# Performance work log

Hardware: AMD Instinct MI355X
Metric: run time of the kernel (lower is better)

## Reference

```python
import jax, jax.numpy as jnp
import numpy as np

B = 128; D = 192; DI = 384; DS = 16; DR = 12; L = 17; DEPTH = 12
NH = 8; HD = D // NH; NCLS = 10; EPS = 1e-5


def setup_inputs() -> dict:
    key = jax.random.key(0)
    ks = iter(jax.random.split(key, 128))
    def rn(shape, s=0.02):
        return jax.random.normal(next(ks), shape, dtype=jnp.float32) * s
    inp = {"x": jax.random.normal(next(ks), (B, 8, 224, 16), dtype=jnp.float32)}
    inp["t_patch_w"] = rn((D, 8, 14, 16)); inp["t_patch_b"] = jnp.zeros((D,), jnp.float32)
    inp["f_patch_w"] = rn((D, 8, 224, 1)); inp["f_patch_b"] = jnp.zeros((D,), jnp.float32)
    inp["t_tok"] = rn((1, 1, D)); inp["f_tok"] = rn((1, 1, D))
    inp["t_pos"] = rn((1, L, D)); inp["f_pos"] = rn((1, L, D))
    for p in ("t", "f"):
        inp[p + "_norm_w"] = jnp.ones((DEPTH, D), jnp.float32)
        inp[p + "_in_proj"] = rn((DEPTH, 2 * DI, D))
        inp[p + "_conv_w"] = rn((DEPTH, DI, 4), 0.3)
        inp[p + "_conv_b"] = jnp.zeros((DEPTH, DI), jnp.float32)
        inp[p + "_x_proj"] = rn((DEPTH, DR + 2 * DS, DI))
        inp[p + "_dt_w"] = rn((DEPTH, DI, DR))
        inp[p + "_dt_b"] = rn((DEPTH, DI), 0.5)
        A = jnp.tile(jnp.arange(1, DS + 1, dtype=jnp.float32)[None, None, :], (DEPTH, DI, 1))
        inp[p + "_A_log"] = jnp.log(A)
        inp[p + "_D"] = jnp.ones((DEPTH, DI), jnp.float32)
        inp[p + "_out_proj"] = rn((DEPTH, D, DI))
    inp["att_t_w"] = rn((4, D, D)); inp["att_t_b"] = jnp.zeros((4, D), jnp.float32)
    inp["att_tf_w"] = rn((4, D, D)); inp["att_tf_b"] = jnp.zeros((4, D), jnp.float32)
    inp["cls1_w"] = rn((512, D)); inp["cls1_b"] = jnp.zeros((512,), jnp.float32)
    inp["cls2_w"] = rn((NCLS, 512)); inp["cls2_b"] = jnp.zeros((NCLS,), jnp.float32)
    inp["pos1_w"] = rn((512, D)); inp["pos1_b"] = jnp.zeros((512,), jnp.float32)
    inp["pos2_w"] = rn((3, 512)); inp["pos2_b"] = jnp.zeros((3,), jnp.float32)
    return inp


def silu(x):
    return x * jax.nn.sigmoid(x)


def patch_embed(x, w, b, stride):
    # Conv2d VALID, then flatten(2).transpose(1,2) -> (B, num_patch, D)
    y = jax.lax.conv_general_dilated(x, w, window_strides=stride, padding="VALID",
                                     dimension_numbers=("NCHW", "OIHW", "NCHW"))
    y = y + b[None, :, None, None]
    Bb, C, H, W = y.shape
    return y.reshape(Bb, C, H * W).transpose(0, 2, 1)


def rmsnorm(x, w):
    return x * jax.lax.rsqrt(jnp.mean(x * x, -1, keepdims=True) + EPS) * w


def mamba_mixer(x, in_proj, conv_w, conv_b, x_proj, dt_w, dt_b, A_log, Dp, out_proj):
    Bb, Ll, _ = x.shape
    xz = x @ in_proj.T                         # (B,L,2*DI)
    xx, z = xz[..., :DI], xz[..., DI:]
    # depthwise causal conv, kernel 4, left pad 3
    xp = jnp.pad(xx, ((0, 0), (3, 0), (0, 0)))
    xx = sum(xp[:, k:k + Ll, :] * conv_w[:, k] for k in range(4)) + conv_b
    xx = silu(xx)                              # (B,L,DI)
    dbl = xx @ x_proj.T                        # (B,L,DR+2*DS)
    dt = jax.nn.softplus(dbl[..., :DR] @ dt_w.T + dt_b)     # (B,L,DI)
    Bm = dbl[..., DR:DR + DS]                  # (B,L,DS)
    Cm = dbl[..., DR + DS:]                    # (B,L,DS)
    A = -jnp.exp(A_log)                        # (DI,DS)
    dA = jnp.exp(dt[..., None] * A)            # (B,L,DI,DS)
    dBx = dt[..., None] * Bm[:, :, None, :] * xx[..., None]

    def step(h, inputs):
        dA_l, dBx_l, C_l = inputs
        h = dA_l * h + dBx_l
        y = jnp.einsum("bcn,bn->bc", h, C_l)
        return h, y

    h0 = jnp.zeros((Bb, DI, DS), x.dtype)
    _, ys = jax.lax.scan(step, h0, (dA.transpose(1, 0, 2, 3),
                                    dBx.transpose(1, 0, 2, 3),
                                    Cm.transpose(1, 0, 2)))
    y = ys.transpose(1, 0, 2) + Dp * xx
    y = y * silu(z)
    return y @ out_proj.T


def backbone(x, norm_w, in_proj, conv_w, conv_b, x_proj, dt_w, dt_b, A_log, Dp, out_proj):
    residual = None
    for i in range(DEPTH):
        residual = x if residual is None else residual + x
        h = rmsnorm(residual, norm_w[i])
        x = mamba_mixer(h, in_proj[i], conv_w[i], conv_b[i], x_proj[i],
                        dt_w[i], dt_b[i], A_log[i], Dp[i], out_proj[i])
    return x


def cross_attn(q, kv, w, b):
    Bb, Lq, _ = q.shape; Lk = kv.shape[1]
    qh = (q @ w[0].T + b[0]).reshape(Bb, Lq, NH, HD).transpose(0, 2, 1, 3)
    kh = (kv @ w[1].T + b[1]).reshape(Bb, Lk, NH, HD).transpose(0, 2, 1, 3)
    vh = (kv @ w[2].T + b[2]).reshape(Bb, Lk, NH, HD).transpose(0, 2, 1, 3)
    att = jax.nn.softmax(jnp.einsum("bhqd,bhkd->bhqk", qh, kh) / np.float32(np.sqrt(HD)), axis=-1)
    o = jnp.einsum("bhqk,bhkd->bhqd", att, vh).transpose(0, 2, 1, 3).reshape(Bb, Lq, D)
    return o @ w[3].T + b[3]


def reference(x, t_patch_w, t_patch_b, f_patch_w, f_patch_b, t_tok, f_tok, t_pos, f_pos,
              t_norm_w, t_in_proj, t_conv_w, t_conv_b, t_x_proj, t_dt_w, t_dt_b, t_A_log, t_D, t_out_proj,
              f_norm_w, f_in_proj, f_conv_w, f_conv_b, f_x_proj, f_dt_w, f_dt_b, f_A_log, f_D, f_out_proj,
              att_t_w, att_t_b, att_tf_w, att_tf_b,
              cls1_w, cls1_b, cls2_w, cls2_b, pos1_w, pos1_b, pos2_w, pos2_b):
    Bb = x.shape[0]
    t = patch_embed(x, t_patch_w, t_patch_b, (14, 1))     # (B,16,D)
    f = patch_embed(x, f_patch_w, f_patch_b, (1, 1))      # (B,16,D)
    t = jnp.concatenate([t, jnp.broadcast_to(t_tok, (Bb, 1, D))], axis=1)
    f = jnp.concatenate([f, jnp.broadcast_to(f_tok, (Bb, 1, D))], axis=1)
    t = t + t_pos
    f = f + f_pos
    t = backbone(t, t_norm_w, t_in_proj, t_conv_w, t_conv_b, t_x_proj,
                 t_dt_w, t_dt_b, t_A_log, t_D, t_out_proj)
    f = backbone(f, f_norm_w, f_in_proj, f_conv_w, f_conv_b, f_x_proj,
                 f_dt_w, f_dt_b, f_A_log, f_D, f_out_proj)
    t1 = cross_attn(t, f, att_t_w, att_t_b)
    fusion = cross_attn(t1, f, att_tf_w, att_tf_b)
    fusion = t + fusion
    feat = fusion[:, -1, :]
    cls = jax.nn.relu(feat @ cls1_w.T + cls1_b) @ cls2_w.T + cls2_b
    pos = jax.nn.relu(feat @ pos1_w.T + pos1_b) @ pos2_w.T + pos2_b
    return (cls, pos)
```

## Files before the change

### kernel.cpp

```cpp
#include <hip/hip_runtime.h>
#include <math.h>

#define NB 128
#define SEQ 17
#define DM 192
#define DI 384
#define DEPTH 12
#define ROW (SEQ*DM)
#define NROWS 4352
#define N192 (NROWS*DM)
#define C1IP (DEPTH*2*DI*DM)
#define C2OP (DEPTH*DM*DI)
#define KEMB 1792
#define CEMB_STRIDE 786432

typedef __attribute__((ext_vector_type(8))) short bf16x8;
typedef __attribute__((ext_vector_type(4))) float f32x4;

struct MambaW {
  const float* norm_w;
  const float* in_proj;
  const float* conv_w;
  const float* conv_b;
  const float* x_proj;
  const float* dt_w;
  const float* dt_b;
  const float* A_log;
  const float* D;
  const float* out_proj;
};

__device__ __forceinline__ float dot4(float4 a, float4 b) {
  return a.x*b.x + a.y*b.y + a.z*b.z + a.w*b.w;
}
__device__ __forceinline__ unsigned short f2bf(float f) {
  unsigned int u = __float_as_uint(f);
  u += 0x7FFFu + ((u >> 16) & 1u);
  return (unsigned short)(u >> 16);
}
__device__ __forceinline__ float bf2f(unsigned short h) {
  return __uint_as_float(((unsigned int)h) << 16);
}
__device__ __forceinline__ void split2(float v, unsigned short& h, unsigned short& l) {
  h = f2bf(v);
  l = f2bf(v - bf2f(h));
}

__global__ __launch_bounds__(256) void decomp_kernel(
    const float* __restrict__ s0, const float* __restrict__ s1,
    unsigned short* __restrict__ hi, unsigned short* __restrict__ lo, int nquads)
{
  const float* s = blockIdx.y ? s1 : s0;
  size_t base = (size_t)blockIdx.y * nquads;
  for (size_t i = (size_t)blockIdx.x*256 + threadIdx.x; i < (size_t)nquads;
       i += (size_t)gridDim.x*256) {
    float4 v = ((const float4*)s)[i];
    ushort4 h, l;
    split2(v.x, h.x, l.x); split2(v.y, h.y, l.y);
    split2(v.z, h.z, l.z); split2(v.w, h.w, l.w);
    ((ushort4*)hi)[base + i] = h;
    ((ushort4*)lo)[base + i] = l;
  }
}

__global__ __launch_bounds__(256) void prep_kernel(
    const float* __restrict__ x, float* __restrict__ Af)
{
  const int t = threadIdx.x;
  const int b = blockIdx.x >> 3, c = blockIdx.x & 7;
  const float* xp = x + (size_t)(b*8 + c)*3584;
  __shared__ float ts[16][225];
  for (int idx = t; idx < 3584; idx += 256)
    ts[idx & 15][idx >> 4] = xp[idx];
  __syncthreads();
  for (int i4 = t; i4 < 896; i4 += 256) {
    const int p = i4 / 56, r4 = (i4 - p*56)*4;
    float4 v;
    v.x = ts[p][r4]; v.y = ts[p][r4+1]; v.z = ts[p][r4+2]; v.w = ts[p][r4+3];
    *(float4*)&Af[(size_t)(b*16 + p)*KEMB + c*224 + r4] = v;
  }
}

__global__ __launch_bounds__(256) void gemm_embed(
    const float* __restrict__ x, const float* __restrict__ Af,
    const float* __restrict__ Wt, const float* __restrict__ Wf,
    float* __restrict__ C)
{
  const int t = threadIdx.x;
  const int mt = blockIdx.x, nt = blockIdx.y, kz = blockIdx.z;
  __shared__ float As[32][68];
  __shared__ float Bs[32][68];

  const float* Wsel = (nt < 32 ? Wt : Wf) + (size_t)(mt*64)*KEMB;

  const int srow = t >> 2;
  const int a8   = t & 3;
  const int sw   = (a8 & 1) << 4;
  const int colA = srow ^ sw;

  const int tn = t & 15;
  const int tm = t >> 4;
  float acc[4][4];
#pragma unroll
  for (int i = 0; i < 4; ++i)
#pragma unroll
    for (int j = 0; j < 4; ++j) acc[i][j] = 0.f;

  const int kbase = kz*448;
  const float* xrowbase = nullptr;
  const float* afrow    = nullptr;
  if (nt < 32) {
    const int r = nt*64 + srow;
    const int b = r >> 4, p = r & 15;
    xrowbase = x + (size_t)(b*8)*3584 + p*224 + a8*8;
  } else {
    const int r = (nt - 32)*64 + srow;
    afrow = Af + (size_t)r*KEMB + kbase + a8*8;
  }
  const float* brow = Wsel + (size_t)srow*KEMB + kbase + a8*8;

  int cblk = kz*2, rr = 0;
  float4 pa0, pa1, pb0, pb1;
  {
    const float* ar = (nt < 32) ? (xrowbase + (size_t)cblk*3584 + rr) : afrow;
    pa0 = *(const float4*)(ar + 0);
    pa1 = *(const float4*)(ar + 4);
    pb0 = *(const float4*)(brow + 0);
    pb1 = *(const float4*)(brow + 4);
  }

  for (int kt = 0; kt < 448; kt += 32) {
    As[a8*8+0][colA]=pa0.x; As[a8*8+1][colA]=pa0.y;
    As[a8*8+2][colA]=pa0.z; As[a8*8+3][colA]=pa0.w;
    As[a8*8+4][colA]=pa1.x; As[a8*8+5][colA]=pa1.y;
    As[a8*8+6][colA]=pa1.z; As[a8*8+7][colA]=pa1.w;
    Bs[a8*8+0][colA]=pb0.x; Bs[a8*8+1][colA]=pb0.y;
    Bs[a8*8+2][colA]=pb0.z; Bs[a8*8+3][colA]=pb0.w;
    Bs[a8*8+4][colA]=pb1.x; Bs[a8*8+5][colA]=pb1.y;
    Bs[a8*8+6][colA]=pb1.z; Bs[a8*8+7][colA]=pb1.w;
    __syncthreads();
    if (kt + 32 < 448) {
      rr += 32; if (rr == 224) { rr = 0; ++cblk; }
      const float* ar = (nt < 32) ? (xrowbase + (size_t)cblk*3584 + rr)
                                  : (afrow + kt + 32);
      pa0 = *(const float4*)(ar + 0);
      pa1 = *(const float4*)(ar + 4);
      const float* br = brow + kt + 32;
      pb0 = *(const float4*)(br + 0);
      pb1 = *(const float4*)(br + 4);
    }
#pragma unroll
    for (int kk = 0; kk < 32; ++kk) {
      const int xr = ((kk >> 3) & 1) << 4;
      float a[4], b[4];
      *(float4*)&a[0] = *(const float4*)&As[kk][(tn*4) ^ xr];
      *(float4*)&b[0] = *(const float4*)&Bs[kk][(tm*4) ^ xr];
#pragma unroll
      for (int i = 0; i < 4; ++i)
#pragma unroll
        for (int j = 0; j < 4; ++j) acc[i][j] = fmaf(a[i], b[j], acc[i][j]);
    }
    __syncthreads();
  }

  float* Cb = C + (size_t)kz*CEMB_STRIDE
            + (size_t)(nt*64 + tn*4)*DM + mt*64 + tm*4;
#pragma unroll
  for (int i = 0; i < 4; ++i)
    *(float4*)(Cb + (size_t)i*DM) = *(float4*)&acc[i][0];
}

template<int MT>
__global__ __launch_bounds__(256) void gemm_mfma(
    const unsigned short* __restrict__ Ahi, const unsigned short* __restrict__ Alo, int lda,
    const unsigned short* __restrict__ BtHi, const unsigned short* __restrict__ BtLo,
    const unsigned short* __restrict__ BfHi, const unsigned short* __restrict__ BfLo,
    int ldb, int kchunk, float* __restrict__ C, int ldc, long ckstride)
{
  const int t = threadIdx.x;
  const int mt = blockIdx.x, nt = blockIdx.y, kz = blockIdx.z;
  __shared__ alignas(16) unsigned short sAh[64*40], sAl[64*40];
  __shared__ alignas(16) unsigned short sBh[MT*40], sBl[MT*40];

  const bool isT = (nt < 34);
  const unsigned short* aH = Ahi + (size_t)(nt*64)*lda + kz*kchunk;
  const unsigned short* aL = Alo + (size_t)(nt*64)*lda + kz*kchunk;
  const unsigned short* bH = (isT ? BtHi : BfHi) + (size_t)(mt*MT)*ldb + kz*kchunk;
  const unsigned short* bL = (isT ? BtLo : BfLo) + (size_t)(mt*MT)*ldb + kz*kchunk;

  const int wave = t >> 6, lane = t & 63;
  const int arow = wave*16 + (lane & 15);
  const int kb   = (lane >> 4) * 8;

  f32x4 acc[MT/16];
#pragma unroll
  for (int mb = 0; mb < MT/16; ++mb) acc[mb] = (f32x4){0.f, 0.f, 0.f, 0.f};

  const int srow = t >> 2, sseg = (t & 3) * 8;

  for (int kt = 0; kt < kchunk; kt += 32) {
    __syncthreads();
    *(uint4*)(sAh + srow*40 + sseg) = *(const uint4*)(aH + (size_t)srow*lda + kt + sseg);
    *(uint4*)(sAl + srow*40 + sseg) = *(const uint4*)(aL + (size_t)srow*lda + kt + sseg);
#pragma unroll
    for (int rep = 0; rep < MT/64; ++rep) {
      int r2 = rep*64 + srow;
      *(uint4*)(sBh + r2*40 + sseg) = *(const uint4*)(bH + (size_t)r2*ldb + kt + sseg);
      *(uint4*)(sBl + r2*40 + sseg) = *(const uint4*)(bL + (size_t)r2*ldb + kt + sseg);
    }
    __syncthreads();
    bf16x8 ah = *(const bf16x8*)(sAh + arow*40 + kb);
    bf16x8 al = *(const bf16x8*)(sAl + arow*40 + kb);
#pragma unroll
    for (int mb = 0; mb < MT/16; ++mb) {
      bf16x8 bh = *(const bf16x8*)(sBh + (mb*16 + (lane & 15))*40 + kb);
      bf16x8 bl = *(const bf16x8*)(sBl + (mb*16 + (lane & 15))*40 + kb);
      acc[mb] = __builtin_amdgcn_mfma_f32_16x16x32_bf16(al, bh, acc[mb], 0, 0, 0);
      acc[mb] = __builtin_amdgcn_mfma_f32_16x16x32_bf16(ah, bl, acc[mb], 0, 0, 0);
      acc[mb] = __builtin_amdgcn_mfma_f32_16x16x32_bf16(ah, bh, acc[mb], 0, 0, 0);
    }
  }

  float* Cb = C + (long)kz*ckstride
            + (size_t)(nt*64 + wave*16 + (lane >> 4)*4)*ldc + mt*MT + (lane & 15);
#pragma unroll
  for (int mb = 0; mb < MT/16; ++mb)
#pragma unroll
    for (int r = 0; r < 4; ++r)
      Cb[(size_t)r*ldc + mb*16] = acc[mb][r];
}

__global__ __launch_bounds__(192) void embed_fin_kernel(
    const float* __restrict__ Cg,
    const float* __restrict__ bT, const float* __restrict__ posT,
    const float* __restrict__ tokT, const float* __restrict__ nwT,
    const float* __restrict__ bF, const float* __restrict__ posF,
    const float* __restrict__ tokF, const float* __restrict__ nwF,
    float* __restrict__ res,
    unsigned short* __restrict__ hHi, unsigned short* __restrict__ hLo)
{
  const int d = threadIdx.x;
  const int sb = blockIdx.x;
  const int is_f = sb >> 7, b = sb & 127;
  const float* bias = is_f ? bF : bT;
  const float* pos  = is_f ? posF : posT;
  const float* tok  = is_f ? tokF : tokT;
  const float* nw   = is_f ? nwF : nwT;
  __shared__ float sq[SEQ*192];
  __shared__ float pt[SEQ*8];
  __shared__ float sc[SEQ];

  float v[SEQ];
  const float* Crow = Cg + ((size_t)is_f*2048 + (size_t)b*16)*DM + d;
  const float add = bias[d];
#pragma unroll
  for (int l = 0; l < 16; ++l) {
    v[l] = (Crow[l*DM] + Crow[(size_t)CEMB_STRIDE + l*DM])
         + (Crow[(size_t)2*CEMB_STRIDE + l*DM] + Crow[(size_t)3*CEMB_STRIDE + l*DM])
         + add + pos[l*DM + d];
    sq[l*192 + d] = v[l]*v[l];
  }
  v[16] = tok[d] + pos[16*DM + d];
  sq[16*192 + d] = v[16]*v[16];
  __syncthreads();
  if (d < 136) {
    int l = d >> 3, j = d & 7;
    float s = 0.f;
#pragma unroll
    for (int q = 0; q < 24; ++q) s += sq[l*192 + j + 8*q];
    pt[d] = s;
  }
  __syncthreads();
  if (d < SEQ) {
    float s = 0.f;
#pragma unroll
    for (int j = 0; j < 8; ++j) s += pt[d*8 + j];
    sc[d] = rsqrtf(s*(1.0f/192.0f) + 1e-5f);
  }
  __syncthreads();
  float nwd = nw[d];
#pragma unroll
  for (int l = 0; l < SEQ; ++l) {
    size_t idx = ((size_t)sb*SEQ + l)*DM + d;
    res[idx] = v[l];
    unsigned short h, lo_;
    split2(v[l]*sc[l]*nwd, h, lo_);
    hHi[idx] = h; hLo[idx] = lo_;
  }
}

__global__ __launch_bounds__(384) void mid_kernel(
    const float* __restrict__ xzg,
    unsigned short* __restrict__ yHi, unsigned short* __restrict__ yLo,
    MambaW wt, MambaW wf, int layer)
{
  const int t = threadIdx.x;
  const int sb = blockIdx.x;
  const MambaW W = (sb >= NB) ? wf : wt;
  __shared__ alignas(16) float lds_xx[SEQ*388];
  __shared__ alignas(16) float lds_dbl[748];
  const size_t nb = (size_t)sb*SEQ;

  float xr[SEQ];
  {
    const float4 cw = ((const float4*)(W.conv_w + (size_t)layer*DI*4))[t];
    const float cb = W.conv_b[layer*DI + t];
    float p0 = 0.f, p1 = 0.f, p2 = 0.f;
#pragma unroll
    for (int l = 0; l < SEQ; ++l) {
      float xz = xzg[(nb + l)*768 + t];
      float v = cb + xz*cw.w + p0*cw.z + p1*cw.y + p2*cw.x;
      p2 = p1; p1 = p0; p0 = xz;
      v = v / (1.f + __expf(-v));
      xr[l] = v;
      lds_xx[l*388 + t] = v;
    }
  }
  __syncthreads();

  {
    const float* XP = W.x_proj + (size_t)layer*44*DI;
#pragma unroll
    for (int rep = 0; rep < 2; ++rep) {
      int o = t + rep*384;
      if (o < 748) {
        int j = o / 17, l = o - j*17;
        const float4* wr = (const float4*)(XP + j*DI);
        const float4* xv4 = (const float4*)lds_xx + l*97;
        float a = 0.f;
        for (int k4 = 0; k4 < 96; ++k4) a += dot4(xv4[k4], wr[k4]);
        lds_dbl[l*44 + j] = a;
      }
    }
  }
  __syncthreads();

  {
    const int c = t;
    const float* dwr = W.dt_w + (size_t)layer*DI*12 + c*12;
    float w0[12];
#pragma unroll
    for (int r = 0; r < 12; ++r) w0[r] = dwr[r];
    const float dtb = W.dt_b[layer*DI + c];
    const float4* alr = (const float4*)(W.A_log + (size_t)layer*DI*16) + c*4;
    float Av[16];
#pragma unroll
    for (int q = 0; q < 4; ++q) {
      float4 a4 = alr[q];
      Av[q*4+0] = -__expf(a4.x); Av[q*4+1] = -__expf(a4.y);
      Av[q*4+2] = -__expf(a4.z); Av[q*4+3] = -__expf(a4.w);
    }
    const float Dp = W.D[layer*DI + c];
    float hst[16];
#pragma unroll
    for (int n = 0; n < 16; ++n) hst[n] = 0.f;
    for (int l = 0; l < SEQ; ++l) {
      float a = dtb;
#pragma unroll
      for (int r = 0; r < 12; ++r) a += lds_dbl[l*44 + r]*w0[r];
      float dt = (a > 20.f) ? a : log1pf(__expf(a));
      float xv = xr[l];
      const float4* dbv = (const float4*)(lds_dbl + l*44 + 12);
      float4 Bq[4], Cq[4];
      Bq[0]=dbv[0]; Bq[1]=dbv[1]; Bq[2]=dbv[2]; Bq[3]=dbv[3];
      Cq[0]=dbv[4]; Cq[1]=dbv[5]; Cq[2]=dbv[6]; Cq[3]=dbv[7];
      const float* Bs = (const float*)Bq;
      const float* Cs = (const float*)Cq;
      float y = 0.f;
      float dbx = dt * xv;
#pragma unroll
      for (int n = 0; n < 16; ++n) {
        float dA = __expf(dt * Av[n]);
        float hn = dA*hst[n] + dbx*Bs[n];
        hst[n] = hn;
        y += hn*Cs[n];
      }
      y += Dp * xv;
      float zv = xzg[(nb + l)*768 + DI + c];
      y *= zv / (1.f + __expf(-zv));
      unsigned short h, lo_;
      split2(y, h, lo_);
      size_t idx = (nb + l)*DI + c;
      yHi[idx] = h; yLo[idx] = lo_;
    }
  }
}

__global__ __launch_bounds__(192) void fuse_kernel(
    const float* __restrict__ part, float* __restrict__ res,
    unsigned short* __restrict__ hHi, unsigned short* __restrict__ hLo,
    float* __restrict__ xfin,
    const float* __restrict__ nwT, const float* __restrict__ nwF,
    int layer, int last)
{
  const int d = threadIdx.x;
  const int sb = blockIdx.x;
  const size_t nb = (size_t)sb*SEQ;
  __shared__ float sq[SEQ*192];
  __shared__ float pt[SEQ*8];
  __shared__ float sc[SEQ];

  float v[SEQ];
#pragma unroll
  for (int l = 0; l < SEQ; ++l) {
    size_t idx = (nb + l)*DM + d;
    float s = part[idx] + part[(size_t)N192 + idx];
    if (!last) {
      s += res[idx];
      res[idx] = s;
      v[l] = s;
      sq[l*192 + d] = s*s;
    } else {
      xfin[idx] = s;
    }
  }
  if (last) return;
  __syncthreads();
  if (d < 136) {
    int l = d >> 3, j = d & 7;
    float s = 0.f;
#pragma unroll
    for (int q = 0; q < 24; ++q) s += sq[l*192 + j + 8*q];
    pt[d] = s;
  }
  __syncthreads();
  if (d < SEQ) {
    float s = 0.f;
#pragma unroll
    for (int j = 0; j < 8; ++j) s += pt[d*8 + j];
    sc[d] = rsqrtf(s*(1.0f/192.0f) + 1e-5f);
  }
  __syncthreads();
  const float* nw = ((sb < NB) ? nwT : nwF) + (size_t)(layer + 1)*DM;
  float nwd = nw[d];
#pragma unroll
  for (int l = 0; l < SEQ; ++l) {
    unsigned short h, lo_;
    split2(v[l]*sc[l]*nwd, h, lo_);
    size_t idx = (nb + l)*DM + d;
    hHi[idx] = h; hLo[idx] = lo_;
  }
}

__global__ __launch_bounds__(256, 3) void gemm_kv(
    const float* __restrict__ A, int lda, int ktot,
    const float* __restrict__ Bt, const float* __restrict__ Bf, int ldb,
    const float* __restrict__ bias1, const float* __restrict__ bias2,
    float* __restrict__ C, int ldc)
{
  const int t  = threadIdx.x;
  const int mt = blockIdx.x, nt = blockIdx.y;
  __shared__ float As[32][132];
  __shared__ float Bs[32][100];

  int pass = mt >> 2, kv = (mt >> 1) & 1, half = mt & 1;
  const float* Bp = (pass ? Bf : Bt) + (size_t)(1+kv)*DM*DM + (size_t)(half*96)*ldb;
  const float* bp = (pass ? bias2 : bias1) + (1+kv)*DM + half*96;
  const float* Ap = A + (size_t)(nt*128)*lda;

  const int tn = t & 15, tm = t >> 4;
  float acc[8][6];
#pragma unroll
  for (int i = 0; i < 8; ++i)
#pragma unroll
    for (int j = 0; j < 6; ++j) acc[i][j] = 0.f;

  const int srow = t >> 1;
  const int skl  = (t & 1) * 16;

  for (int kt = 0; kt < ktot; kt += 32) {
    __syncthreads();
    {
      const float* ar = Ap + (size_t)srow*lda + kt + skl;
      float4 v0 = *(const float4*)(ar + 0);
      float4 v1 = *(const float4*)(ar + 4);
      float4 v2 = *(const float4*)(ar + 8);
      float4 v3 = *(const float4*)(ar + 12);
      As[skl+ 0][srow]=v0.x; As[skl+ 1][srow]=v0.y; As[skl+ 2][srow]=v0.z; As[skl+ 3][srow]=v0.w;
      As[skl+ 4][srow]=v1.x; As[skl+ 5][srow]=v1.y; As[skl+ 6][srow]=v1.z; As[skl+ 7][srow]=v1.w;
      As[skl+ 8][srow]=v2.x; As[skl+ 9][srow]=v2.y; As[skl+10][srow]=v2.z; As[skl+11][srow]=v2.w;
      As[skl+12][srow]=v3.x; As[skl+13][srow]=v3.y; As[skl+14][srow]=v3.z; As[skl+15][srow]=v3.w;
    }
    if (srow < 96) {
      const float* br = Bp + (size_t)srow*ldb + kt + skl;
      float4 v0 = *(const float4*)(br + 0);
      float4 v1 = *(const float4*)(br + 4);
      float4 v2 = *(const float4*)(br + 8);
      float4 v3 = *(const float4*)(br + 12);
      Bs[skl+ 0][srow]=v0.x; Bs[skl+ 1][srow]=v0.y; Bs[skl+ 2][srow]=v0.z; Bs[skl+ 3][srow]=v0.w;
      Bs[skl+ 4][srow]=v1.x; Bs[skl+ 5][srow]=v1.y; Bs[skl+ 6][srow]=v1.z; Bs[skl+ 7][srow]=v1.w;
      Bs[skl+ 8][srow]=v2.x; Bs[skl+ 9][srow]=v2.y; Bs[skl+10][srow]=v2.z; Bs[skl+11][srow]=v2.w;
      Bs[skl+12][srow]=v3.x; Bs[skl+13][srow]=v3.y; Bs[skl+14][srow]=v3.z; Bs[skl+15][srow]=v3.w;
    }
    __syncthreads();
#pragma unroll
    for (int kk = 0; kk < 32; ++kk) {
      float a[8], b[6];
      *(float4*)&a[0] = *(const float4*)&As[kk][tn*4];
      *(float4*)&a[4] = *(const float4*)&As[kk][64 + tn*4];
      *(float2*)&b[0] = *(const float2*)&Bs[kk][tm*6];
      *(float2*)&b[2] = *(const float2*)&Bs[kk][tm*6+2];
      *(float2*)&b[4] = *(const float2*)&Bs[kk][tm*6+4];
#pragma unroll
      for (int i = 0; i < 8; ++i)
#pragma unroll
        for (int j = 0; j < 6; ++j) acc[i][j] = fmaf(a[i], b[j], acc[i][j]);
    }
  }

  float* Cb = C + (size_t)(nt*128)*ldc + mt*96;
#pragma unroll
  for (int ni = 0; ni < 8; ++ni) {
    int n = (ni < 4) ? tn*4 + ni : 64 + tn*4 + (ni - 4);
    float* cr = Cb + (size_t)n*ldc;
#pragma unroll
    for (int j = 0; j < 6; ++j) cr[tm*6 + j] = acc[ni][j] + bp[tm*6 + j];
  }
}

__device__ __forceinline__ void coop_gemv192(
    const float* __restrict__ W, const float* __restrict__ bias,
    const float* __restrict__ xv, float* __restrict__ y,
    const float* __restrict__ addv, int nout, int relu,
    float* __restrict__ wbuf, float* __restrict__ pt, int t)
{
  float4 pv[12];
#pragma unroll
  for (int i = 0; i < 12; ++i) pv[i] = *(const float4*)(W + (t + i*256)*4);
  for (int d0 = 0; d0 < nout; d0 += 64) {
#pragma unroll
    for (int i = 0; i < 12; ++i) {
      const int idx = (t + i*256)*4;
      const int r = idx/192, c = idx - r*192;
      float* wb = wbuf + r*193 + c;
      wb[0]=pv[i].x; wb[1]=pv[i].y; wb[2]=pv[i].z; wb[3]=pv[i].w;
    }
    __syncthreads();
    if (d0 + 64 < nout) {
      const float* nsrc = W + (size_t)(d0+64)*192;
#pragma unroll
      for (int i = 0; i < 12; ++i) pv[i] = *(const float4*)(nsrc + (t + i*256)*4);
    }
    {
      const int ol = t & 63, ks = t >> 6;
      const float* wr = wbuf + ol*193 + ks*48;
      const float* xr = xv + ks*48;
      float a = 0.f;
#pragma unroll
      for (int k = 0; k < 48; ++k) a = fmaf(wr[k], xr[k], a);
      pt[ks*64 + ol] = a;
    }
    __syncthreads();
    if (t < 64) {
      float s = (pt[t] + pt[64+t]) + (pt[128+t] + pt[192+t]) + bias[d0+t];
      if (addv) s += addv[d0+t];
      if (relu) s = fmaxf(s, 0.f);
      y[d0+t] = s;
    }
    __syncthreads();
  }
}

__global__ __launch_bounds__(256) void attn_core_kernel(
    const float* __restrict__ xfin, const float* __restrict__ kvg,
    const float* __restrict__ w1, const float* __restrict__ b1,
    const float* __restrict__ w2, const float* __restrict__ b2,
    const float* __restrict__ c1w, const float* __restrict__ c1b,
    const float* __restrict__ c2w, const float* __restrict__ c2b,
    const float* __restrict__ p1w, const float* __restrict__ p1b,
    const float* __restrict__ p2w, const float* __restrict__ p2b,
    float* __restrict__ out)
{
  const int t = threadIdx.x;
  const int b = blockIdx.x >> 1;
  const int path = blockIdx.x & 1;
  __shared__ float wbuf[64*193];
  __shared__ float pt[256];
  __shared__ float pth[256];
  __shared__ alignas(16) float t16[DM];
  __shared__ alignas(16) float qv[DM];
  __shared__ alignas(16) float ov[DM];
  __shared__ alignas(16) float t1[DM];
  __shared__ alignas(16) float feat[DM];
  __shared__ alignas(16) float hbuf[512];

  if (t < DM) t16[t] = xfin[((size_t)b*SEQ + 16)*DM + t];
  __syncthreads();

  for (int pass = 0; pass < 2; ++pass) {
    const float* wa = pass ? w2 : w1;
    const float* ba = pass ? b2 : b1;
    coop_gemv192(wa, ba, pass ? t1 : t16, qv, nullptr, DM, 0, wbuf, pt, t);
    if (t < DM) {
      int h = t / 24;
      float4 q0 = *(const float4*)&qv[h*24];
      float4 q1 = *(const float4*)&qv[h*24+4];
      float4 q2 = *(const float4*)&qv[h*24+8];
      float4 q3 = *(const float4*)&qv[h*24+12];
      float4 q4 = *(const float4*)&qv[h*24+16];
      float4 q5 = *(const float4*)&qv[h*24+20];
      float scs[SEQ];
      float mx = -1e30f;
#pragma unroll
      for (int lk = 0; lk < SEQ; ++lk) {
        const float4* kr = (const float4*)(kvg + ((size_t)b*SEQ + lk)*768 + pass*384 + h*24);
        float s_ = dot4(q0,kr[0]) + dot4(q1,kr[1]) + dot4(q2,kr[2])
                 + dot4(q3,kr[3]) + dot4(q4,kr[4]) + dot4(q5,kr[5]);
        s_ *= 0.20412414523193154f;
        scs[lk] = s_;
        mx = fmaxf(mx, s_);
      }
      float den = 0.f;
#pragma unroll
      for (int lk = 0; lk < SEQ; ++lk) { float e = __expf(scs[lk]-mx); scs[lk]=e; den += e; }
      float inv = 1.f/den;
      float o = 0.f;
#pragma unroll
      for (int lk = 0; lk < SEQ; ++lk)
        o += scs[lk] * kvg[((size_t)b*SEQ + lk)*768 + pass*384 + DM + t];
      ov[t] = o*inv;
    }
    __syncthreads();
    coop_gemv192(wa + 3*DM*DM, ba + 3*DM, ov, pass ? feat : t1,
                 pass ? t16 : nullptr, DM, 0, wbuf, pt, t);
  }

  coop_gemv192(path ? p1w : c1w, path ? p1b : c1b, feat, hbuf,
               nullptr, 512, 1, wbuf, pt, t);

  {
    const int op = t & 15, ks = t >> 4;
    const int nop = path ? 3 : 10;
    float a = 0.f;
    if (op < nop) {
      const float* wr = (path ? p2w : c2w) + (size_t)op*512 + ks*32;
      const float4* w4 = (const float4*)wr;
      const float4* v4 = (const float4*)(hbuf + ks*32);
#pragma unroll
      for (int j = 0; j < 8; ++j) a += dot4(v4[j], w4[j]);
    }
    pth[op*16 + ks] = a;
  }
  __syncthreads();
  if (t < (path ? 3 : 10)) {
    float s = 0.f;
#pragma unroll
    for (int j = 0; j < 16; ++j) s += pth[t*16 + j];
    if (!path) out[b*10 + t] = s + c2b[t];
    else       out[1280 + b*3 + t] = s + p2b[t];
  }
}

extern "C" void kernel_launch(void* const* d_in, const int* in_sizes, int n_in,
                              void* d_out, int out_size, void* d_ws, size_t ws_size,
                              hipStream_t stream)
{
  (void)in_sizes; (void)n_in; (void)out_size; (void)ws_size;
  const float* x    = (const float*)d_in[0];
  const float* tpw  = (const float*)d_in[1];
  const float* tpb  = (const float*)d_in[2];
  const float* fpw  = (const float*)d_in[3];
  const float* fpb  = (const float*)d_in[4];
  const float* ttok = (const float*)d_in[5];
  const float* ftok = (const float*)d_in[6];
  const float* tpos = (const float*)d_in[7];
  const float* fpos = (const float*)d_in[8];
  MambaW wt { (const float*)d_in[9],  (const float*)d_in[10], (const float*)d_in[11],
              (const float*)d_in[12], (const float*)d_in[13], (const float*)d_in[14],
              (const float*)d_in[15], (const float*)d_in[16], (const float*)d_in[17],
              (const float*)d_in[18] };
  MambaW wf { (const float*)d_in[19], (const float*)d_in[20], (const float*)d_in[21],
              (const float*)d_in[22], (const float*)d_in[23], (const float*)d_in[24],
              (const float*)d_in[25], (const float*)d_in[26], (const float*)d_in[27],
              (const float*)d_in[28] };
  const float* attw  = (const float*)d_in[29];
  const float* attb  = (const float*)d_in[30];
  const float* attw2 = (const float*)d_in[31];
  const float* attb2 = (const float*)d_in[32];
  const float* c1w = (const float*)d_in[33];
  const float* c1b = (const float*)d_in[34];
  const float* c2w = (const float*)d_in[35];
  const float* c2b = (const float*)d_in[36];
  const float* p1w = (const float*)d_in[37];
  const float* p1b = (const float*)d_in[38];
  const float* p2w = (const float*)d_in[39];
  const float* p2b = (const float*)d_in[40];

  float* ws = (float*)d_ws;
  size_t off = 0;
  float* res  = ws + off; off += (size_t)N192;
  float* xfin = ws + off; off += (size_t)N192;
  float* xzg  = ws + off; off += (size_t)4*N192;
  float* part = ws + off; off += (size_t)2*N192;
  unsigned short* hHi = (unsigned short*)(ws + off); off += (size_t)N192/2;
  unsigned short* hLo = (unsigned short*)(ws + off); off += (size_t)N192/2;
  unsigned short* yHi = (unsigned short*)(ws + off); off += (size_t)N192;
  unsigned short* yLo = (unsigned short*)(ws + off); off += (size_t)N192;
  unsigned short* ipHi = (unsigned short*)(ws + off); off += (size_t)C1IP;
  unsigned short* ipLo = (unsigned short*)(ws + off); off += (size_t)C1IP;
  unsigned short* opHi = (unsigned short*)(ws + off); off += (size_t)C2OP;
  unsigned short* opLo = (unsigned short*)(ws + off); off += (size_t)C2OP;
  float* kvg = part;

  float* Cemb = ws + (size_t)N192;
  float* Af   = ws + (size_t)N192 + (size_t)4*CEMB_STRIDE;

  decomp_kernel<<<dim3(512, 2), 256, 0, stream>>>(wt.in_proj, wf.in_proj,
                                                  ipHi, ipLo, C1IP/4);
  decomp_kernel<<<dim3(512, 2), 256, 0, stream>>>(wt.out_proj, wf.out_proj,
                                                  opHi, opLo, C2OP/4);
  prep_kernel<<<1024, 256, 0, stream>>>(x, Af);
  gemm_embed<<<dim3(3, 64, 4), 256, 0, stream>>>(x, Af, tpw, fpw, Cemb);
  embed_fin_kernel<<<256, 192, 0, stream>>>(Cemb,
      tpb, tpos, ttok, wt.norm_w,
      fpb, fpos, ftok, wf.norm_w,
      res, hHi, hLo);

  for (int i = 0; i < DEPTH; ++i) {
    const size_t ipo = (size_t)i*2*DI*DM;
    const size_t opo = (size_t)i*DM*DI;
    gemm_mfma<128><<<dim3(6, 68, 1), 256, 0, stream>>>(
        hHi, hLo, DM,
        ipHi + ipo, ipLo + ipo, ipHi + C1IP + ipo, ipLo + C1IP + ipo,
        DM, DM , xzg, 768, 0);
    mid_kernel<<<256, 384, 0, stream>>>(xzg, yHi, yLo, wt, wf, i);
    gemm_mfma<64><<<dim3(3, 68, 2), 256, 0, stream>>>(
        yHi, yLo, DI,
        opHi + opo, opLo + opo, opHi + C2OP + opo, opLo + C2OP + opo,
        DI, 192, part, DM, (long)N192);
    fuse_kernel<<<256, 192, 0, stream>>>(part, res, hHi, hLo, xfin,
        wt.norm_w, wf.norm_w, i, (i == DEPTH-1) ? 1 : 0);
  }

  gemm_kv<<<dim3(8, 17), 256, 0, stream>>>(
      xfin + (size_t)NB*ROW, DM, DM,
      attw, attw2, DM, attb, attb2, kvg, 768);
  attn_core_kernel<<<256, 256, 0, stream>>>(xfin, kvg,
      attw, attb, attw2, attb2,
      c1w, c1b, c2w, c2b, p1w, p1b, p2w, p2b, (float*)d_out);
}
```

Baseline: 1.199 ms.

## Remap embed GEMM blocks per XCD, shrink in_proj tile, rework gemv staging

The embed GEMM now uses a flat 1D grid and maps block IDs so that blocks on the same XCD (block index mod 8) share N and K tiles, aiming for better per-XCD L2 reuse. The per-layer in_proj GEMM moves from a 128-wide to a 64-wide tile with twice as many blocks, raising occupancy and parallelism at the cost of more A-operand reloads. The cooperative GEMV swaps float4 weight loads for scalar coalesced loads and strided shared-memory stores, removing the per-element div/mod and likely cutting shared-memory bank conflicts, though it issues more load instructions and holds 48 registers per thread.

```diff
diff --git a/kernel.cpp b/kernel.cpp
--- a/kernel.cpp
+++ b/kernel.cpp
@@ -87,7 +87,15 @@
     float* __restrict__ C)
 {
   const int t = threadIdx.x;
-  const int mt = blockIdx.x, nt = blockIdx.y, kz = blockIdx.z;
+  const int bidx = blockIdx.x;
+  const int xcd = bidx & 7;
+  const int s_  = bidx >> 3;
+  const int mt  = s_ % 3;
+  const int u   = s_ / 3;
+  const int trio = xcd*32 + u;
+  const int nt  = trio & 63;
+  const int kz  = trio >> 6;
+
   __shared__ float As[32][68];
   __shared__ float Bs[32][68];
 
@@ -524,22 +532,29 @@
     const float* __restrict__ addv, int nout, int relu,
     float* __restrict__ wbuf, float* __restrict__ pt, int t)
 {
-  float4 pv[12];
-#pragma unroll
-  for (int i = 0; i < 12; ++i) pv[i] = *(const float4*)(W + (t + i*256)*4);
+  float pv[48];
+#pragma unroll
+  for (int i = 0; i < 48; ++i) pv[i] = W[t + i*256];
   for (int d0 = 0; d0 < nout; d0 += 64) {
-#pragma unroll
-    for (int i = 0; i < 12; ++i) {
-      const int idx = (t + i*256)*4;
-      const int r = idx/192, c = idx - r*192;
-      float* wb = wbuf + r*193 + c;
-      wb[0]=pv[i].x; wb[1]=pv[i].y; wb[2]=pv[i].z; wb[3]=pv[i].w;
+    {
+      int r0 = t / 192;
+      int c0 = t - r0*192;
+      int addr = r0*193 + c0;
+      int c = c0;
+#pragma unroll
+      for (int i = 0; i < 48; ++i) {
+        wbuf[addr] = pv[i];
+        c += 64;
+        const int wrap = (c >= 192);
+        c -= wrap ? 192 : 0;
+        addr += wrap ? 258 : 257;
+      }
     }
     __syncthreads();
     if (d0 + 64 < nout) {
       const float* nsrc = W + (size_t)(d0+64)*192;
 #pragma unroll
-      for (int i = 0; i < 12; ++i) pv[i] = *(const float4*)(nsrc + (t + i*256)*4);
+      for (int i = 0; i < 48; ++i) pv[i] = nsrc[t + i*256];
     }
     {
       const int ol = t & 63, ks = t >> 6;
@@ -710,7 +725,7 @@
   decomp_kernel<<<dim3(512, 2), 256, 0, stream>>>(wt.out_proj, wf.out_proj,
                                                   opHi, opLo, C2OP/4);
   prep_kernel<<<1024, 256, 0, stream>>>(x, Af);
-  gemm_embed<<<dim3(3, 64, 4), 256, 0, stream>>>(x, Af, tpw, fpw, Cemb);
+  gemm_embed<<<768, 256, 0, stream>>>(x, Af, tpw, fpw, Cemb);
   embed_fin_kernel<<<256, 192, 0, stream>>>(Cemb,
       tpb, tpos, ttok, wt.norm_w,
       fpb, fpos, ftok, wf.norm_w,
@@ -719,7 +734,7 @@
   for (int i = 0; i < DEPTH; ++i) {
     const size_t ipo = (size_t)i*2*DI*DM;
     const size_t opo = (size_t)i*DM*DI;
-    gemm_mfma<128><<<dim3(6, 68, 1), 256, 0, stream>>>(
+    gemm_mfma<64><<<dim3(12, 68, 1), 256, 0, stream>>>(
         hHi, hLo, DM,
         ipHi + ipo, ipLo + ipo, ipHi + C1IP + ipo, ipLo + C1IP + ipo,
         DM, DM , xzg, 768, 0);
```

New measurement: 1.137 ms. 5.2% less time.
